# Kernel tuning notes

Hardware: AMD Instinct MI355X
Metric: run time of the kernel (lower is better)

## Reference

```python
import jax, jax.numpy as jnp
import numpy as np

B, F, D, A = 1024, 33, 128, 128  # batch, num_fields, embed_dim, attn_size (A must equal gnn dim)

def setup_inputs() -> dict:
    key = jax.random.key(0)
    k1, k2, k3, k4 = jax.random.split(key, 4)
    gnn_feature = jax.random.normal(k1, (B, A), dtype=jnp.float32)
    x = jax.random.normal(k2, (B, F, D), dtype=jnp.float32)
    # attention Linear(embed_dim -> attn_size): weight (A, D), bias (A,)
    lim = 1.0 / np.sqrt(D)
    attn_W = jax.random.uniform(k3, (A, D), minval=-lim, maxval=lim, dtype=jnp.float32)
    attn_b = jax.random.uniform(k4, (A,), minval=-lim, maxval=lim, dtype=jnp.float32)
    return {"gnn_feature": gnn_feature, "x": x, "attn_W": attn_W, "attn_b": attn_b}

def reference(gnn_feature, x, attn_W, attn_b):
    num_fields = x.shape[1]
    row, col = np.triu_indices(num_fields, k=1)  # P = F*(F-1)/2 pairs
    inner = x[:, row] * x[:, col]                # [B, P, D]
    fm = jax.nn.relu(jnp.einsum('bpd,ad->bpa', inner, attn_W) + attn_b)  # [B, P, A]
    # bmm(gnn[b,1,A], fm[b,p,A,1]) -> dot product per pair, softmax over pairs
    scores = jnp.einsum('ba,bpa->bp', gnn_feature, fm)  # [B, P]
    attn = jax.nn.softmax(scores, axis=1)               # [B, P]
    attn_output = jnp.einsum('bp,bpd->bd', attn, inner) * 100.0  # [B, D]
    return jnp.concatenate([gnn_feature, attn_output], axis=1)   # [B, A+D]
```

## Files before the change

### kernel.cpp

```cpp
#include <hip/hip_runtime.h>

#define FN 33
#define DN 128
#define AN 128
#define PN 528
#define MTN 33
#define XS 136
#define AS 36
#define SS 544

typedef __attribute__((ext_vector_type(8))) _Float16 half8;
typedef __attribute__((ext_vector_type(2))) _Float16 h2;
typedef __attribute__((ext_vector_type(4))) float f32x4;
typedef __attribute__((ext_vector_type(2))) float f32x2;
typedef __attribute__((ext_vector_type(4))) unsigned int u32x4;

__device__ __forceinline__ unsigned int pkrtz(float a, float b) {
  return __builtin_bit_cast(unsigned int, __builtin_amdgcn_cvt_pkrtz(a, b));
}
__device__ __forceinline__ h2 ash2(unsigned int u) { return __builtin_bit_cast(h2, u); }

__device__ __forceinline__ float row_sum16(float v) {
  v += __builtin_bit_cast(float, __builtin_amdgcn_update_dpp(0, __builtin_bit_cast(int, v), 0x128, 0xF, 0xF, false));
  v += __builtin_bit_cast(float, __builtin_amdgcn_update_dpp(0, __builtin_bit_cast(int, v), 0x124, 0xF, 0xF, false));
  v += __builtin_bit_cast(float, __builtin_amdgcn_update_dpp(0, __builtin_bit_cast(int, v), 0x122, 0xF, 0xF, false));
  v += __builtin_bit_cast(float, __builtin_amdgcn_update_dpp(0, __builtin_bit_cast(int, v), 0x121, 0xF, 0xF, false));
  return v;
}

__global__ __launch_bounds__(256, 3)
void afm_kernel(const float* __restrict__ gnn, const float* __restrict__ xg,
                const float* __restrict__ Wg,  const float* __restrict__ bg,
                float* __restrict__ out)
{
  __shared__ __align__(16) _Float16 xh[FN * XS];
  __shared__ __align__(16) unsigned int attn_h2[FN * AS];
  __shared__ __align__(16) float scores2[2 * SS];
  __shared__ __align__(16) float part[512];
  __shared__ unsigned short rowcol[PN];

  const int tid  = threadIdx.x;
  const int b    = blockIdx.x;
  const int wave = tid >> 6;
  const int lane = tid & 63;
  const int q    = lane >> 4;
  const int u    = lane & 15;
  const int mh   = wave >> 1;
  const int nh   = wave & 1;

  for (int p = tid; p < PN; p += 256) {
    int i = 0, rem = p;
    while (rem >= FN - 1 - i) { rem -= FN - 1 - i; i++; }
    rowcol[p] = (unsigned short)(i | ((i + 1 + rem) << 8));
  }
  const f32x4* xg4 = (const f32x4*)(xg + (size_t)b * FN * DN);
  for (int idx = tid; idx < (FN * DN) / 4; idx += 256) {
    f32x4 v = xg4[idx];
    int i  = idx >> 5;
    int d0 = (idx & 31) << 2;
    *(uint2*)&xh[i * XS + d0] = make_uint2(pkrtz(v.x, v.y), pkrtz(v.z, v.w));
  }
  for (int idx = tid; idx < FN * AS; idx += 256) attn_h2[idx] = 0u;

  half8 Bf[4][4];
  #pragma unroll
  for (int nn = 0; nn < 4; nn++) {
    const float* wrow = Wg + (size_t)((nh * 4 + nn) * 16 + u) * DN + q * 8;
    #pragma unroll
    for (int kk = 0; kk < 4; kk++) {
      f32x4 w0 = *(const f32x4*)(wrow + kk * 32);
      f32x4 w1 = *(const f32x4*)(wrow + kk * 32 + 4);
      union { half8 h; unsigned int w[4]; } t;
      t.w[0] = pkrtz(w0.x, w0.y);
      t.w[1] = pkrtz(w0.z, w0.w);
      t.w[2] = pkrtz(w1.x, w1.y);
      t.w[3] = pkrtz(w1.z, w1.w);
      Bf[nn][kk] = t.h;
      asm volatile("" : "+v"(Bf[nn][kk]));
    }
  }
  float garr[4];
  f32x4 bias_acc[4];
  #pragma unroll
  for (int nn = 0; nn < 4; nn++) {
    const int a = (nh * 4 + nn) * 16 + u;
    garr[nn] = gnn[(size_t)b * AN + a];
    float bv = bg[a];
    bias_acc[nn] = (f32x4){bv, bv, bv, bv};
    asm volatile("" : "+v"(garr[nn]), "+v"(bias_acc[nn]));
  }
  __syncthreads();

  {
    int mt = mh;
    unsigned int rc = rowcol[mt * 16 + u];
    int r = rc & 255, c = rc >> 8;
    half8 xr[4], xc[4];
    #pragma unroll
    for (int kk = 0; kk < 4; kk++) {
      xr[kk] = *(const half8*)&xh[r * XS + kk * 32 + q * 8];
      xc[kk] = *(const half8*)&xh[c * XS + kk * 32 + q * 8];
    }
    for (;;) {
      f32x4 acc[4];
      #pragma unroll
      for (int kk = 0; kk < 4; kk++) {
        half8 Af = xr[kk] * xc[kk];
        #pragma unroll
        for (int nn = 0; nn < 4; nn++)
          acc[nn] = __builtin_amdgcn_mfma_f32_16x16x32_f16(
              Af, Bf[nn][kk], kk == 0 ? bias_acc[nn] : acc[nn], 0, 0, 0);
      }

      const int nmt = mt + 2;
      if (nmt < MTN) {
        rc = rowcol[nmt * 16 + u];
        r = rc & 255; c = rc >> 8;
        #pragma unroll
        for (int kk = 0; kk < 4; kk++) {
          xr[kk] = *(const half8*)&xh[r * XS + kk * 32 + q * 8];
          xc[kk] = *(const half8*)&xh[c * XS + kk * 32 + q * 8];
        }
      }

      float sc[4] = {0.f, 0.f, 0.f, 0.f};
      #pragma unroll
      for (int nn = 0; nn < 4; nn++)
        #pragma unroll
        for (int rr = 0; rr < 4; rr++) {
          float fmv = fmaxf(acc[nn][rr], 0.f);
          sc[rr] = fmaf(fmv, garr[nn], sc[rr]);
        }
      #pragma unroll
      for (int rr = 0; rr < 4; rr++) sc[rr] = row_sum16(sc[rr]);
      if (u == 0)
        *(f32x4*)&scores2[nh * SS + mt * 16 + q * 4] = (f32x4){sc[0], sc[1], sc[2], sc[3]};

      if (nmt >= MTN) break;
      mt = nmt;
    }
  }
  __syncthreads();

  float s[9], e[9];
  #pragma unroll
  for (int t = 0; t < 8; t++)
    s[t] = scores2[t * 64 + lane] + scores2[SS + t * 64 + lane];
  s[8] = (lane < 16) ? (scores2[512 + lane] + scores2[SS + 512 + lane]) : -3.4e38f;
  float m = s[0];
  #pragma unroll
  for (int t = 1; t < 9; t++) m = fmaxf(m, s[t]);
  #pragma unroll
  for (int off = 32; off >= 1; off >>= 1) m = fmaxf(m, __shfl_xor(m, off, 64));
  float lsum = 0.f;
  #pragma unroll
  for (int t = 0; t < 9; t++) {
    e[t] = (t == 8 && lane >= 16) ? 0.f : __expf(s[t] - m);
    lsum += e[t];
  }
  #pragma unroll
  for (int off = 32; off >= 1; off >>= 1) lsum += __shfl_xor(lsum, off, 64);
  const float Z = lsum;

  #pragma unroll
  for (int t = 0; t < 9; t++) {
    bool mine = (t < 8) ? ((t >> 1) == wave) : (wave == 3 && lane < 16);
    if (mine) {
      unsigned int rc = rowcol[t * 64 + lane];
      attn_h2[(rc & 255) * AS + ((rc >> 8) - (rc & 255) - 1)] = pkrtz(e[t], e[t]);
    }
  }
  __syncthreads();

  {
    unsigned int xp[36];
    #pragma unroll
    for (int j = 0; j < FN; j++) xp[j] = *(const unsigned int*)&xh[j * XS + 2 * lane];
    xp[33] = 0u; xp[34] = 0u; xp[35] = 0u;

    float a0 = 0.f, a1 = 0.f;
    #pragma unroll
    for (int i = 0; i < 32; i++) {
      if ((i & 3) != wave) continue;
      const int L  = 32 - i;
      const int n4 = (L + 3) >> 2;
      h2 ti2 = (h2)0.0f;
      #pragma unroll
      for (int t = 0; t < 8; t++) {
        if (t >= n4) break;
        u32x4 a4 = *(const u32x4*)&attn_h2[i * AS + 4 * t];
        ti2 += ash2(a4.x) * ash2(xp[i + 1 + 4 * t + 0]);
        ti2 += ash2(a4.y) * ash2(xp[i + 1 + 4 * t + 1]);
        ti2 += ash2(a4.z) * ash2(xp[i + 1 + 4 * t + 2]);
        ti2 += ash2(a4.w) * ash2(xp[i + 1 + 4 * t + 3]);
      }
      h2 xi = ash2(xp[i]);
      a0 = fmaf((float)xi[0], (float)ti2[0], a0);
      a1 = fmaf((float)xi[1], (float)ti2[1], a1);
    }
    *(f32x2*)&part[wave * 128 + 2 * lane] = (f32x2){a0, a1};
  }
  __syncthreads();
  if (tid < DN) {
    float tot = (part[tid] + part[128 + tid]) + (part[256 + tid] + part[384 + tid]);
    out[(size_t)b * (AN + DN) + AN + tid] = tot * (100.0f / Z);
  } else {
    const int a = tid - 128;
    out[(size_t)b * (AN + DN) + a] = gnn[(size_t)b * AN + a];
  }
}

extern "C" void kernel_launch(void* const* d_in, const int* in_sizes, int n_in,
                              void* d_out, int out_size, void* d_ws, size_t ws_size,
                              hipStream_t stream) {
  (void)n_in; (void)out_size; (void)d_ws; (void)ws_size;
  const float* gnn  = (const float*)d_in[0];
  const float* x    = (const float*)d_in[1];
  const float* W    = (const float*)d_in[2];
  const float* bias = (const float*)d_in[3];
  float* out = (float*)d_out;
  const int Bn = in_sizes[0] / AN;
  afm_kernel<<<dim3(Bn), dim3(256), 0, stream>>>(gnn, x, W, bias, out);
}
```

Before: 109.6 us.

## Split fused AFM kernel into score and weighted-sum kernels via workspace

Splits the single fused kernel in two. The first computes the pair scores, with each wave covering all 128 attention columns over its own M-tiles. It writes the scores to a global workspace. The second kernel runs the softmax and the attention-weighted sum, re-reading x from global memory. Pair row/col indices now come from a closed-form sqrt formula instead of a loop. The change aims to shorten per-block shared-memory and register pressure so each phase gets better occupancy. In exchange it pays an extra launch, a global round-trip for the scores, a second read of x, and 8x4 B fragments held in registers.

```diff
diff --git a/kernel.cpp b/kernel.cpp
--- a/kernel.cpp
+++ b/kernel.cpp
@@ -7,7 +7,7 @@
 #define MTN 33
 #define XS 136
 #define AS 36
-#define SS 544
+#define SWS 544
 
 typedef __attribute__((ext_vector_type(8))) _Float16 half8;
 typedef __attribute__((ext_vector_type(2))) _Float16 h2;
@@ -19,6 +19,15 @@
   return __builtin_bit_cast(unsigned int, __builtin_amdgcn_cvt_pkrtz(a, b));
 }
 __device__ __forceinline__ h2 ash2(unsigned int u) { return __builtin_bit_cast(h2, u); }
+
+__device__ __forceinline__ int pair_row(int p, int* jout) {
+  float s = __builtin_sqrtf((float)(4225 - 8 * p));
+  int i = (int)((65.0f - s) * 0.5f);
+  if ((i * (65 - i)) >> 1 > p) i--;
+  if (((i + 1) * (64 - i)) >> 1 <= p) i++;
+  *jout = i + 1 + (p - ((i * (65 - i)) >> 1));
+  return i;
+}
 
 __device__ __forceinline__ float row_sum16(float v) {
   v += __builtin_bit_cast(float, __builtin_amdgcn_update_dpp(0, __builtin_bit_cast(int, v), 0x128, 0xF, 0xF, false));
@@ -28,15 +37,12 @@
   return v;
 }
 
-__global__ __launch_bounds__(256, 3)
-void afm_kernel(const float* __restrict__ gnn, const float* __restrict__ xg,
+__global__ __launch_bounds__(256, 2)
+void afm_scores(const float* __restrict__ gnn, const float* __restrict__ xg,
                 const float* __restrict__ Wg,  const float* __restrict__ bg,
-                float* __restrict__ out)
+                float* __restrict__ sws)
 {
   __shared__ __align__(16) _Float16 xh[FN * XS];
-  __shared__ __align__(16) unsigned int attn_h2[FN * AS];
-  __shared__ __align__(16) float scores2[2 * SS];
-  __shared__ __align__(16) float part[512];
   __shared__ unsigned short rowcol[PN];
 
   const int tid  = threadIdx.x;
@@ -45,13 +51,10 @@
   const int lane = tid & 63;
   const int q    = lane >> 4;
   const int u    = lane & 15;
-  const int mh   = wave >> 1;
-  const int nh   = wave & 1;
 
   for (int p = tid; p < PN; p += 256) {
-    int i = 0, rem = p;
-    while (rem >= FN - 1 - i) { rem -= FN - 1 - i; i++; }
-    rowcol[p] = (unsigned short)(i | ((i + 1 + rem) << 8));
+    int j; int i = pair_row(p, &j);
+    rowcol[p] = (unsigned short)(i | (j << 8));
   }
   const f32x4* xg4 = (const f32x4*)(xg + (size_t)b * FN * DN);
   for (int idx = tid; idx < (FN * DN) / 4; idx += 256) {
@@ -60,12 +63,11 @@
     int d0 = (idx & 31) << 2;
     *(uint2*)&xh[i * XS + d0] = make_uint2(pkrtz(v.x, v.y), pkrtz(v.z, v.w));
   }
-  for (int idx = tid; idx < FN * AS; idx += 256) attn_h2[idx] = 0u;
-
-  half8 Bf[4][4];
-  #pragma unroll
-  for (int nn = 0; nn < 4; nn++) {
-    const float* wrow = Wg + (size_t)((nh * 4 + nn) * 16 + u) * DN + q * 8;
+
+  half8 Bf[8][4];
+  #pragma unroll
+  for (int n = 0; n < 8; n++) {
+    const float* wrow = Wg + (size_t)(n * 16 + u) * DN + q * 8;
     #pragma unroll
     for (int kk = 0; kk < 4; kk++) {
       f32x4 w0 = *(const f32x4*)(wrow + kk * 32);
@@ -75,78 +77,74 @@
       t.w[1] = pkrtz(w0.z, w0.w);
       t.w[2] = pkrtz(w1.x, w1.y);
       t.w[3] = pkrtz(w1.z, w1.w);
-      Bf[nn][kk] = t.h;
-      asm volatile("" : "+v"(Bf[nn][kk]));
-    }
-  }
-  float garr[4];
-  f32x4 bias_acc[4];
-  #pragma unroll
-  for (int nn = 0; nn < 4; nn++) {
-    const int a = (nh * 4 + nn) * 16 + u;
-    garr[nn] = gnn[(size_t)b * AN + a];
-    float bv = bg[a];
-    bias_acc[nn] = (f32x4){bv, bv, bv, bv};
-    asm volatile("" : "+v"(garr[nn]), "+v"(bias_acc[nn]));
+      Bf[n][kk] = t.h;
+      asm volatile("" : "+v"(Bf[n][kk]));
+    }
+  }
+  float garr[8];
+  f32x4 bias_acc[8];
+  #pragma unroll
+  for (int n = 0; n < 8; n++) {
+    garr[n] = gnn[(size_t)b * AN + n * 16 + u];
+    float bv = bg[n * 16 + u];
+    bias_acc[n] = (f32x4){bv, bv, bv, bv};
   }
   __syncthreads();
 
-  {
-    int mt = mh;
-    unsigned int rc = rowcol[mt * 16 + u];
-    int r = rc & 255, c = rc >> 8;
+  for (int mt = wave; mt < MTN; mt += 4) {
+    const unsigned int rc = rowcol[mt * 16 + u];
+    const int r = rc & 255, c = rc >> 8;
     half8 xr[4], xc[4];
     #pragma unroll
     for (int kk = 0; kk < 4; kk++) {
       xr[kk] = *(const half8*)&xh[r * XS + kk * 32 + q * 8];
       xc[kk] = *(const half8*)&xh[c * XS + kk * 32 + q * 8];
     }
-    for (;;) {
-      f32x4 acc[4];
+    f32x4 acc[8];
+    #pragma unroll
+    for (int kk = 0; kk < 4; kk++) {
+      half8 Af = xr[kk] * xc[kk];
       #pragma unroll
-      for (int kk = 0; kk < 4; kk++) {
-        half8 Af = xr[kk] * xc[kk];
-        #pragma unroll
-        for (int nn = 0; nn < 4; nn++)
-          acc[nn] = __builtin_amdgcn_mfma_f32_16x16x32_f16(
-              Af, Bf[nn][kk], kk == 0 ? bias_acc[nn] : acc[nn], 0, 0, 0);
+      for (int n = 0; n < 8; n++)
+        acc[n] = __builtin_amdgcn_mfma_f32_16x16x32_f16(
+            Af, Bf[n][kk], kk == 0 ? bias_acc[n] : acc[n], 0, 0, 0);
+    }
+    float sc[4] = {0.f, 0.f, 0.f, 0.f};
+    #pragma unroll
+    for (int n = 0; n < 8; n++)
+      #pragma unroll
+      for (int rr = 0; rr < 4; rr++) {
+        float fmv = fmaxf(acc[n][rr], 0.f);
+        sc[rr] = fmaf(fmv, garr[n], sc[rr]);
       }
-
-      const int nmt = mt + 2;
-      if (nmt < MTN) {
-        rc = rowcol[nmt * 16 + u];
-        r = rc & 255; c = rc >> 8;
-        #pragma unroll
-        for (int kk = 0; kk < 4; kk++) {
-          xr[kk] = *(const half8*)&xh[r * XS + kk * 32 + q * 8];
-          xc[kk] = *(const half8*)&xh[c * XS + kk * 32 + q * 8];
-        }
-      }
-
-      float sc[4] = {0.f, 0.f, 0.f, 0.f};
-      #pragma unroll
-      for (int nn = 0; nn < 4; nn++)
-        #pragma unroll
-        for (int rr = 0; rr < 4; rr++) {
-          float fmv = fmaxf(acc[nn][rr], 0.f);
-          sc[rr] = fmaf(fmv, garr[nn], sc[rr]);
-        }
-      #pragma unroll
-      for (int rr = 0; rr < 4; rr++) sc[rr] = row_sum16(sc[rr]);
-      if (u == 0)
-        *(f32x4*)&scores2[nh * SS + mt * 16 + q * 4] = (f32x4){sc[0], sc[1], sc[2], sc[3]};
-
-      if (nmt >= MTN) break;
-      mt = nmt;
-    }
-  }
-  __syncthreads();
-
+    #pragma unroll
+    for (int rr = 0; rr < 4; rr++) sc[rr] = row_sum16(sc[rr]);
+    if (u == 0)
+      *(f32x4*)&sws[(size_t)b * SWS + mt * 16 + q * 4] = (f32x4){sc[0], sc[1], sc[2], sc[3]};
+  }
+}
+
+__global__ __launch_bounds__(128, 4)
+void afm_out(const float* __restrict__ gnn, const float* __restrict__ xg,
+             const float* __restrict__ sws, float* __restrict__ out)
+{
+  __shared__ __align__(16) unsigned int attn_h2[FN * AS];
+  __shared__ __align__(16) float part[256];
+
+  const int tid  = threadIdx.x;
+  const int b    = blockIdx.x;
+  const int wave = tid >> 6;
+  const int lane = tid & 63;
+
+  #pragma unroll
+  for (int r = 0; r < 16; r++)
+    if (lane < AS) attn_h2[(wave + 2 * r) * AS + lane] = 0u;
+
+  const float* srow = sws + (size_t)b * SWS;
   float s[9], e[9];
   #pragma unroll
-  for (int t = 0; t < 8; t++)
-    s[t] = scores2[t * 64 + lane] + scores2[SS + t * 64 + lane];
-  s[8] = (lane < 16) ? (scores2[512 + lane] + scores2[SS + 512 + lane]) : -3.4e38f;
+  for (int t = 0; t < 8; t++) s[t] = srow[t * 64 + lane];
+  s[8] = (lane < 16) ? srow[512 + lane] : -3.4e38f;
   float m = s[0];
   #pragma unroll
   for (int t = 1; t < 9; t++) m = fmaxf(m, s[t]);
@@ -164,61 +162,60 @@
 
   #pragma unroll
   for (int t = 0; t < 9; t++) {
-    bool mine = (t < 8) ? ((t >> 1) == wave) : (wave == 3 && lane < 16);
-    if (mine) {
-      unsigned int rc = rowcol[t * 64 + lane];
-      attn_h2[(rc & 255) * AS + ((rc >> 8) - (rc & 255) - 1)] = pkrtz(e[t], e[t]);
-    }
-  }
+    if (t == 8 && lane >= 16) continue;
+    int p = t * 64 + lane;
+    int j; int i = pair_row(p, &j);
+    if ((i & 1) == wave)
+      attn_h2[i * AS + (j - i - 1)] = pkrtz(e[t], e[t]);
+  }
+
+  unsigned int xp[36];
+  #pragma unroll
+  for (int j = 0; j < FN; j++) {
+    f32x2 v = *(const f32x2*)&xg[((size_t)b * FN + j) * DN + 2 * lane];
+    xp[j] = pkrtz(v.x, v.y);
+  }
+  xp[33] = 0u; xp[34] = 0u; xp[35] = 0u;
+
+  float a0 = 0.f, a1 = 0.f;
+  #pragma unroll
+  for (int i = 0; i < 32; i++) {
+    if ((i & 1) != wave) continue;
+    const int L  = 32 - i;
+    const int n4 = (L + 3) >> 2;
+    h2 ti2 = (h2)0.0f;
+    #pragma unroll
+    for (int t = 0; t < 8; t++) {
+      if (t >= n4) break;
+      u32x4 a4 = *(const u32x4*)&attn_h2[i * AS + 4 * t];
+      ti2 += ash2(a4.x) * ash2(xp[i + 1 + 4 * t + 0]);
+      ti2 += ash2(a4.y) * ash2(xp[i + 1 + 4 * t + 1]);
+      ti2 += ash2(a4.z) * ash2(xp[i + 1 + 4 * t + 2]);
+      ti2 += ash2(a4.w) * ash2(xp[i + 1 + 4 * t + 3]);
+    }
+    h2 xi = ash2(xp[i]);
+    a0 = fmaf((float)xi[0], (float)ti2[0], a0);
+    a1 = fmaf((float)xi[1], (float)ti2[1], a1);
+  }
+  *(f32x2*)&part[wave * 128 + 2 * lane] = (f32x2){a0, a1};
   __syncthreads();
 
-  {
-    unsigned int xp[36];
-    #pragma unroll
-    for (int j = 0; j < FN; j++) xp[j] = *(const unsigned int*)&xh[j * XS + 2 * lane];
-    xp[33] = 0u; xp[34] = 0u; xp[35] = 0u;
-
-    float a0 = 0.f, a1 = 0.f;
-    #pragma unroll
-    for (int i = 0; i < 32; i++) {
-      if ((i & 3) != wave) continue;
-      const int L  = 32 - i;
-      const int n4 = (L + 3) >> 2;
-      h2 ti2 = (h2)0.0f;
-      #pragma unroll
-      for (int t = 0; t < 8; t++) {
-        if (t >= n4) break;
-        u32x4 a4 = *(const u32x4*)&attn_h2[i * AS + 4 * t];
-        ti2 += ash2(a4.x) * ash2(xp[i + 1 + 4 * t + 0]);
-        ti2 += ash2(a4.y) * ash2(xp[i + 1 + 4 * t + 1]);
-        ti2 += ash2(a4.z) * ash2(xp[i + 1 + 4 * t + 2]);
-        ti2 += ash2(a4.w) * ash2(xp[i + 1 + 4 * t + 3]);
-      }
-      h2 xi = ash2(xp[i]);
-      a0 = fmaf((float)xi[0], (float)ti2[0], a0);
-      a1 = fmaf((float)xi[1], (float)ti2[1], a1);
-    }
-    *(f32x2*)&part[wave * 128 + 2 * lane] = (f32x2){a0, a1};
-  }
-  __syncthreads();
-  if (tid < DN) {
-    float tot = (part[tid] + part[128 + tid]) + (part[256 + tid] + part[384 + tid]);
-    out[(size_t)b * (AN + DN) + AN + tid] = tot * (100.0f / Z);
-  } else {
-    const int a = tid - 128;
-    out[(size_t)b * (AN + DN) + a] = gnn[(size_t)b * AN + a];
-  }
+  float tot = part[tid] + part[128 + tid];
+  out[(size_t)b * (AN + DN) + tid] = gnn[(size_t)b * AN + tid];
+  out[(size_t)b * (AN + DN) + AN + tid] = tot * (100.0f / Z);
 }
 
 extern "C" void kernel_launch(void* const* d_in, const int* in_sizes, int n_in,
                               void* d_out, int out_size, void* d_ws, size_t ws_size,
                               hipStream_t stream) {
-  (void)n_in; (void)out_size; (void)d_ws; (void)ws_size;
+  (void)n_in; (void)out_size; (void)ws_size;
   const float* gnn  = (const float*)d_in[0];
   const float* x    = (const float*)d_in[1];
   const float* W    = (const float*)d_in[2];
   const float* bias = (const float*)d_in[3];
   float* out = (float*)d_out;
+  float* sws = (float*)d_ws;
   const int Bn = in_sizes[0] / AN;
-  afm_kernel<<<dim3(Bn), dim3(256), 0, stream>>>(gnn, x, W, bias, out);
-}
+  afm_scores<<<dim3(Bn), dim3(256), 0, stream>>>(gnn, x, W, bias, sws);
+  afm_out   <<<dim3(Bn), dim3(128), 0, stream>>>(gnn, x, sws, out);
+}
```

New measurement: 123.0 us. 1.12x slower.
